# Kernel tuning notes

Hardware: AMD Instinct MI355X
Metric: run time of the kernel (lower is better)

Reference implementation:

```python
import jax, jax.numpy as jnp
import numpy as np

B = 2
ROW, COL = 63, 84          # resolution
ROW_, COL_ = 32, 42        # resolution_
N = ROW * COL              # 5292 kv tokens
N_ = ROW_ * COL_           # 1344 q tokens
IN_DIM, OUT_DIM = 256, 512
KEY_DIM, NUM_HEADS, ATTN_RATIO, STRIDE = 16, 8, 2, 2
D = ATTN_RATIO * KEY_DIM   # 32 (value dim per head)
DH = D * NUM_HEADS         # 256
NH_KD = KEY_DIM * NUM_HEADS  # 128
H_KV = DH + NH_KD          # 384
SCALE = KEY_DIM ** -0.5
EPS = 1e-5


def _build_bias_idxs():
    # replicates the itertools.product double loop, vectorized; ids ordered by
    # first occurrence in row-major scan (same as dict insertion order).
    r_ = np.arange(ROW_); c_ = np.arange(COL_)
    r = np.arange(ROW); c = np.arange(COL)
    off_r = np.abs(r_[:, None] * STRIDE - r[None, :])      # (32, 63)
    off_c = np.abs(c_[:, None] * STRIDE - c[None, :])      # (42, 84)
    keys = (off_r[:, None, :, None] * 1000 + off_c[None, :, None, :]).reshape(-1)
    _, first_idx, inv = np.unique(keys, return_index=True, return_inverse=True)
    order = np.argsort(first_idx)
    rank = np.empty_like(order); rank[order] = np.arange(len(order))
    idxs = rank[inv].reshape(N_, N).astype(np.int32)
    return idxs, len(order)


def setup_inputs() -> dict:
    key = jax.random.key(0)
    ks = jax.random.split(key, 12)
    idxs_np, n_off = _build_bias_idxs()
    inp = {
        "x": jax.random.normal(ks[0], (B, N, IN_DIM), jnp.float32),
        "kv_w": jax.random.normal(ks[1], (H_KV, IN_DIM), jnp.float32) * (IN_DIM ** -0.5),
        "kv_g": jnp.ones((H_KV,), jnp.float32),
        "kv_b": jnp.zeros((H_KV,), jnp.float32),
        "q_w": jax.random.normal(ks[2], (NH_KD, IN_DIM), jnp.float32) * (IN_DIM ** -0.5),
        "q_g": jnp.ones((NH_KD,), jnp.float32),
        "q_b": jnp.zeros((NH_KD,), jnp.float32),
        "proj_w": jax.random.normal(ks[3], (OUT_DIM, DH), jnp.float32) * (DH ** -0.5),
        "proj_g": jnp.ones((OUT_DIM,), jnp.float32),
        "proj_b": jnp.zeros((OUT_DIM,), jnp.float32),
        "bias_table": jax.random.normal(ks[4], (NUM_HEADS, n_off), jnp.float32) * 0.02,
        "bias_idxs": jnp.asarray(idxs_np),
    }
    return inp


def _linear_bn(x, w, g, b):
    # Linear (no bias) followed by BatchNorm1d in training mode (batch stats
    # over flattened (B*N) dim, biased variance).
    y = jnp.einsum("bnc,oc->bno", x, w)
    flat = y.reshape(-1, y.shape[-1])
    mu = flat.mean(0)
    var = flat.var(0)
    return (y - mu) * (g / jnp.sqrt(var + EPS)) + b


def _hardswish(x):
    return x * jnp.clip(x + 3.0, 0.0, 6.0) / 6.0


def reference(x, kv_w, kv_g, kv_b, q_w, q_g, q_b, proj_w, proj_g, proj_b,
              bias_table, bias_idxs):
    Bx = x.shape[0]
    # kv projection -> split k (KEY_DIM) and v (D) per head
    kv = _linear_bn(x, kv_w, kv_g, kv_b).reshape(Bx, N, NUM_HEADS, KEY_DIM + D)
    k = kv[..., :KEY_DIM].transpose(0, 2, 1, 3)   # (B, H, N, key_dim)
    v = kv[..., KEY_DIM:].transpose(0, 2, 1, 3)   # (B, H, N, d)
    # q: spatial subsample then projection
    xs = x.reshape(Bx, ROW, COL, IN_DIM)[:, ::STRIDE, ::STRIDE].reshape(Bx, N_, IN_DIM)
    q = _linear_bn(xs, q_w, q_g, q_b).reshape(Bx, N_, NUM_HEADS, KEY_DIM).transpose(0, 2, 1, 3)
    # gathered relative position bias: (H, N_, N)
    ab = bias_table[:, bias_idxs]
    attn = jnp.einsum("bhqd,bhkd->bhqk", q, k) * SCALE + ab[None]
    attn = jax.nn.softmax(attn, axis=-1)
    out = jnp.einsum("bhqk,bhkd->bhqd", attn, v)       # (B, H, N_, d)
    out = out.transpose(0, 2, 1, 3).reshape(Bx, N_, DH)
    out = _linear_bn(_hardswish(out), proj_w, proj_g, proj_b)
    return out
```

## Files before the change

kernel.cpp:

```cpp
#include <hip/hip_runtime.h>
#include <hip/hip_bf16.h>
#include <math.h>

#define N_K 5292
#define N_KP 5376
#define N_Q 1344
#define NH_KD 128
#define NROWS 21504
#define NSPLIT 8
#define LOG2E 1.4426950408889634f
#define MSTAT 16.0f

typedef float f32x4 __attribute__((ext_vector_type(4)));
typedef short short8 __attribute__((ext_vector_type(8)));

__device__ __forceinline__ float fexp2(float x) {
#if __has_builtin(__builtin_amdgcn_exp2f)
    return __builtin_amdgcn_exp2f(x);
#else
    return exp2f(x);
#endif
}

__device__ __forceinline__ unsigned pk_bf16(float a, float b) {
    union { __hip_bfloat162 h; unsigned u; } c;
    c.h = __float22bfloat162_rn(make_float2(a, b));
    return c.u;
}
__device__ __forceinline__ unsigned short f2bf(float a) {
    return (unsigned short)pk_bf16(a, 0.f);
}

__global__ __launch_bounds__(256) void prep_bf16(
    const float* __restrict__ X, const float* __restrict__ kv_w,
    const float* __restrict__ q_w,
    unsigned short* __restrict__ Xb, float* __restrict__ sums)
{
    int i = blockIdx.x * 256 + threadIdx.x;
    if (i >= 710144) {
        int j = i - 710144;
        float4 z = make_float4(0.f, 0.f, 0.f, 0.f);
        *(float4*)(sums + (size_t)j * 8)     = z;
        *(float4*)(sums + (size_t)j * 8 + 4) = z;
        return;
    }
    const float* src;
    long off;
    if (i < 677376)       { src = X;      off = i; }
    else if (i < 701952)  { src = kv_w;   off = i - 677376; }
    else                  { src = q_w;    off = i - 701952; }
    float4 v = *(const float4*)(src + off * 4);
    *(uint2*)(Xb + (size_t)i * 4) = make_uint2(pk_bf16(v.x, v.y), pk_bf16(v.z, v.w));
}

__device__ __forceinline__ void gemm_body_bb(
    const unsigned short* __restrict__ A, const unsigned short* __restrict__ W,
    long asrc, int nrow,
    unsigned short (*As)[40], unsigned short (*Bs)[40], f32x4 acc[4])
{
    const int t = threadIdx.x;
    const int w = t >> 6, lane = t & 63, g = lane >> 4, ln = lane & 15;
    const int srow = t >> 2;
    const int sc8 = (t & 3) * 8;

    for (int k0 = 0; k0 < 256; k0 += 32) {
        uint4 a = make_uint4(0, 0, 0, 0);
        if (asrc >= 0) a = *(const uint4*)(A + asrc * 256 + k0 + sc8);
        uint4 b = *(const uint4*)(W + (size_t)nrow * 256 + k0 + sc8);

        __syncthreads();
        *(uint4*)&As[srow][sc8] = a;
        *(uint4*)&Bs[srow][sc8] = b;
        __syncthreads();

        short8 ah = *(const short8*)&As[w * 16 + ln][g * 8];
        #pragma unroll
        for (int nt = 0; nt < 4; ++nt) {
            short8 bh = *(const short8*)&Bs[nt * 16 + ln][g * 8];
            acc[nt] = __builtin_amdgcn_mfma_f32_16x16x32_bf16(ah, bh, acc[nt], 0, 0, 0);
        }
    }
}

__device__ __forceinline__ void gemm_stats(f32x4 acc[4], float* __restrict__ sums,
                                           int n0, int Ncols, float* scratch)
{
    const int t = threadIdx.x;
    const int w = t >> 6, lane = t & 63, g = lane >> 4, ln = lane & 15;
    float s4[4], q4[4];
    #pragma unroll
    for (int nt = 0; nt < 4; ++nt) {
        float s = acc[nt][0] + acc[nt][1] + acc[nt][2] + acc[nt][3];
        float q = fmaf(acc[nt][0], acc[nt][0], fmaf(acc[nt][1], acc[nt][1],
                  fmaf(acc[nt][2], acc[nt][2], acc[nt][3] * acc[nt][3])));
        s += __shfl_xor(s, 16); s += __shfl_xor(s, 32);
        q += __shfl_xor(q, 16); q += __shfl_xor(q, 32);
        s4[nt] = s; q4[nt] = q;
    }
    __syncthreads();
    float* st_s = scratch;
    float* st_q = scratch + 256;
    if (g == 0) {
        #pragma unroll
        for (int nt = 0; nt < 4; ++nt) {
            st_s[(w * 4 + nt) * 16 + ln] = s4[nt];
            st_q[(w * 4 + nt) * 16 + ln] = q4[nt];
        }
    }
    __syncthreads();
    if (t < 64) {
        int nt = t >> 4, c = t & 15;
        float a = 0.f, b2 = 0.f;
        #pragma unroll
        for (int ww = 0; ww < 4; ++ww) {
            a  += st_s[(ww * 4 + nt) * 16 + c];
            b2 += st_q[(ww * 4 + nt) * 16 + c];
        }
        atomicAdd(&sums[n0 + nt * 16 + c], a);
        atomicAdd(&sums[Ncols + n0 + nt * 16 + c], b2);
    }
}

__global__ __launch_bounds__(256) void gemm_qkv(
    const unsigned short* __restrict__ Xb, const unsigned short* __restrict__ kvWb,
    const unsigned short* __restrict__ qWb,
    const float* __restrict__ bias_table, const int* __restrict__ bias_idxs, int n_off,
    unsigned short* __restrict__ Kp, unsigned short* __restrict__ Vpt,
    float* __restrict__ bt_r,
    float* __restrict__ q_y, float* __restrict__ sums_kv, float* __restrict__ sums_q)
{
    __shared__ unsigned short As[64][40], Bs[64][40];
    const int t = threadIdx.x;
    const int w = t >> 6, lane = t & 63, g = lane >> 4, ln = lane & 15;
    const int srow = t >> 2;
    int id = blockIdx.x;

    if (id >= 1104) {
        id -= 1104;
        if (id < 168) {
            int i = id * 256 + t;
            int row = i / 84, j = i - row * 84;
            int slot;
            if (j < 20) {
                int kap = 44 + j;
                slot = 5248 + (((kap & 15) << 2) | (kap >> 4));
            } else {
                slot = 5312 + (j - 20);
            }
            Vpt[(size_t)row * N_KP + slot] = 0;
        } else {
            int i = (id - 168) * 256 + t;
            if (i < 8 * N_K) {
                int h = i / N_K, j = i - h * N_K;
                bt_r[i] = bias_table[h * n_off + bias_idxs[j]] * LOG2E;
            }
        }
        return;
    }

    f32x4 acc[4];
    #pragma unroll
    for (int nt = 0; nt < 4; ++nt) acc[nt] = (f32x4){0.f, 0.f, 0.f, 0.f};

    if (id < 1008) {
        const int xcd = id & 7, id8 = id >> 3;
        const int my = xcd + (id8 / 6) * 8, ny = id8 % 6;
        if (my >= 166) return;
        const int m0 = my * 64, n0 = ny * 64;
        int mrow = m0 + srow;
        long asrc = (mrow < 10584) ? mrow : -1;
        gemm_body_bb(Xb, kvWb, asrc, n0 + srow, As, Bs, acc);

        #pragma unroll
        for (int nt = 0; nt < 4; ++nt) {
            int c = n0 + nt * 16 + ln;
            int hh = c / 48, cc = c - 48 * hh;
            #pragma unroll
            for (int reg = 0; reg < 4; ++reg) {
                int mr = m0 + w * 16 + g * 4 + reg;
                if (mr < 10584) {
                    int bb = mr >= N_K;
                    int key = mr - bb * N_K;
                    unsigned short v16 = f2bf(acc[nt][reg]);
                    if (cc < 16) {
                        Kp[((size_t)(bb * 8 + hh) * N_K + key) * 16 + cc] = v16;
                    } else {
                        int kap = key & 63;
                        int keyp = (key & ~63) | (((kap & 15) << 2) | (kap >> 4));
                        Vpt[((size_t)(bb * 8 + hh) * 32 + cc - 16) * N_KP + keyp] = v16;
                    }
                }
            }
        }
        gemm_stats(acc, sums_kv, n0, 384, (float*)&As[0][0]);
    } else {
        id -= 1008;
        const int xcd = id & 7, id8 = id >> 3;
        const int my = xcd + (id8 / 2) * 8, ny = id8 % 2;
        if (my >= 42) return;
        const int m0 = my * 64, n0 = ny * 64;
        int mrow = m0 + srow;
        int bb = mrow / N_Q;
        int i = mrow - bb * N_Q;
        long asrc = (long)(bb * N_K + (i / 42) * 168 + (i % 42) * 2);
        gemm_body_bb(Xb, qWb, asrc, n0 + srow, As, Bs, acc);

        #pragma unroll
        for (int nt = 0; nt < 4; ++nt)
            #pragma unroll
            for (int reg = 0; reg < 4; ++reg) {
                int mr = m0 + w * 16 + g * 4 + reg;
                q_y[(size_t)mr * 128 + n0 + nt * 16 + ln] = acc[nt][reg];
            }
        gemm_stats(acc, sums_q, n0, 128, (float*)&As[0][0]);
    }
}

__global__ __launch_bounds__(256) void gemm_proj(
    const unsigned short* __restrict__ Ap, const unsigned short* __restrict__ Wp,
    float* __restrict__ Y, float* __restrict__ sums)
{
    __shared__ unsigned short As[64][40], Bs[64][40];
    const int t = threadIdx.x;
    const int w = t >> 6, lane = t & 63, g = lane >> 4, ln = lane & 15;
    const int id = blockIdx.x;
    const int xcd = id & 7, id8 = id >> 3;
    const int my = xcd + (id8 / 8) * 8, ny = id8 % 8;
    if (my >= 42) return;
    const int m0 = my * 64, n0 = ny * 64;

    f32x4 acc[4];
    #pragma unroll
    for (int nt = 0; nt < 4; ++nt) acc[nt] = (f32x4){0.f, 0.f, 0.f, 0.f};
    gemm_body_bb(Ap, Wp, m0 + (t >> 2), n0 + (t >> 2), As, Bs, acc);

    #pragma unroll
    for (int nt = 0; nt < 4; ++nt)
        #pragma unroll
        for (int reg = 0; reg < 4; ++reg) {
            int mr = m0 + w * 16 + g * 4 + reg;
            Y[(size_t)mr * 512 + n0 + nt * 16 + ln] = acc[nt][reg];
        }
    gemm_stats(acc, sums, n0, 512, (float*)&As[0][0]);
}

__global__ __launch_bounds__(256, 5) void attn_mfma(
    const unsigned short* __restrict__ Kp, const unsigned short* __restrict__ Vpt,
    const float* __restrict__ q_y, const float* __restrict__ sums_q,
    const float* __restrict__ q_g, const float* __restrict__ q_b,
    const float* __restrict__ sums_kv, const float* __restrict__ kv_g,
    const float* __restrict__ bt_r,
    float* __restrict__ pl, float* __restrict__ pacc)
{
    const int id = blockIdx.x;
    const int h = id & 7;
    const int z = (id >> 3) & 15;
    const int qt = id >> 7;
    const int b = z >> 3, ks = z & 7;
    const int t = threadIdx.x;
    const int w = t >> 6, lane = t & 63, g = lane >> 4, ln = lane & 15;

    __shared__ unsigned short btm_s[14 * 166];
    __shared__ unsigned short K_s[2][64][24];
    __shared__ unsigned short Vt_s[2][32][72];
    __shared__ unsigned short P_s[4][16][72];

    const int q0 = qt * 64;
    const int t0 = (ks * 83) >> 3;
    const int t1 = ((ks + 1) * 83) >> 3;
    const int kstart = t0 * 64;
    const int kend0 = t1 * 64;
    const int kend = kend0 < N_K ? kend0 : N_K;
    const int ntiles = t1 - t0;
    const bool tail = (ks == 7);

    const int kr0 = kstart / 84;
    const int kr1 = (kend - 1) / 84;
    const int rq2min = (q0 / 42) * 2;
    const int rq2max = ((q0 + 63) / 42) * 2;
    const int dmin_r = rq2min - kr1;
    const int rows = (rq2max - kr0) - dmin_r + 1;
    const int nb = rows * 166;
    const unsigned mxb = (unsigned)((nb - 1) * 2);
    {
        const float* src = bt_r + h * N_K;
        for (int j = t; j < nb; j += 256) {
            int rr = j / 166, ii = j - rr * 166;
            int dr = dmin_r + rr; dr = dr < 0 ? -dr : dr;
            int dc = ii - 83; dc = dc < 0 ? -dc : dc;
            btm_s[j] = f2bf(src[dr * 84 + dc]);
        }
    }

    short8 qfrag = (short8)0;
    if (lane < 32) {
        const float invq = 1.f / 2688.f, invk = 1.f / 10584.f;
        const float post = 0.25f * LOG2E;
        const int c0 = h * 16 + g * 8;
        const int ck = h * 48 + g * 8;
        const float* qp = q_y + (size_t)(b * N_Q + q0 + w * 16 + ln) * NH_KD + c0;
        float vv[8];
        #pragma unroll
        for (int j = 0; j < 8; ++j) {
            float mu  = sums_q[c0 + j] * invq;
            float var = fmaf(-mu, mu, sums_q[128 + c0 + j] * invq);
            float s   = q_g[c0 + j] * rsqrtf(var + 1e-5f) * post;
            float vq  = fmaf(qp[j], s, fmaf(-mu, s, q_b[c0 + j] * post));
            float muk = sums_kv[ck + j] * invk;
            float vrk = fmaf(-muk, muk, sums_kv[384 + ck + j] * invk);
            float sk  = kv_g[ck + j] * rsqrtf(vrk + 1e-5f);
            vv[j] = vq * sk;
        }
        union { short8 s; unsigned u[4]; } qf;
        qf.u[0] = pk_bf16(vv[0], vv[1]); qf.u[1] = pk_bf16(vv[2], vv[3]);
        qf.u[2] = pk_bf16(vv[4], vv[5]); qf.u[3] = pk_bf16(vv[6], vv[7]);
        qfrag = qf.s;
    }

    union { short8 s; unsigned u[4]; } onef;
    #pragma unroll
    for (int j = 0; j < 4; ++j) onef.u[j] = 0x3F803F80u;
    const short8 ones = onef.s;

    int baseb[4];
    #pragma unroll
    for (int reg = 0; reg < 4; ++reg) {
        int qg = q0 + w * 16 + g * 4 + reg;
        int rq2 = (qg / 42) * 2;
        int cq2 = (qg % 42) * 2;
        baseb[reg] = ((rq2 - dmin_r) * 166 + cq2 + 83) * 2;
    }
    int offb[4], kcc[4];
    #pragma unroll
    for (int st = 0; st < 4; ++st) {
        int kg = kstart + st * 16 + ln;
        int okr = kg / 84;
        kcc[st] = kg - okr * 84;
        offb[st] = -(okr * 166 + kcc[st]) * 2;
    }

    const unsigned* kp_base = (const unsigned*)Kp + (size_t)(b * 8 + h) * N_K * 8;
    const int skey = t >> 2, schunk = t & 3;
    const int vrow = t >> 3, vc8 = (t & 7) * 8;
    const unsigned short* vptr = Vpt + (size_t)(b * 8 + h) * 32 * N_KP
                                     + (size_t)vrow * N_KP + kstart + vc8;

    uint2 kreg; uint4 vreg;
    {
        int kg = kstart + skey; if (kg > N_K - 1) kg = N_K - 1;
        kreg = *(const uint2*)(kp_base + (size_t)kg * 8 + schunk * 2);
        vreg = *(const uint4*)vptr;
    }
    *(uint2*)&K_s[0][skey][schunk * 4] = kreg;
    *(uint4*)&Vt_s[0][vrow][vc8] = vreg;
    __syncthreads();

    f32x4 acc0 = {0.f, 0.f, 0.f, 0.f}, acc1 = {0.f, 0.f, 0.f, 0.f};
    f32x4 accL = {0.f, 0.f, 0.f, 0.f};
    const f32x4 minit = {-MSTAT, -MSTAT, -MSTAT, -MSTAT};
    int p = 0;

    for (int it = 0; it < ntiles; ++it) {
        const int k0 = kstart + it * 64;
        const bool notlast = (it + 1 < ntiles);
        if (notlast) {
            int kg = k0 + 64 + skey; if (kg > N_K - 1) kg = N_K - 1;
            kreg = *(const uint2*)(kp_base + (size_t)kg * 8 + schunk * 2);
            vreg = *(const uint4*)(vptr + 64);
        }

        f32x4 sf[4];
        #pragma unroll
        for (int st = 0; st < 4; ++st) {
            short8 bf = (short8)0;
            if (lane < 32) bf = *(const short8*)&K_s[p][st * 16 + ln][g * 8];
            sf[st] = __builtin_amdgcn_mfma_f32_16x16x32_bf16(qfrag, bf, minit, 0, 0, 0);
        }

        float pv[4][4];
        const bool clampit = tail && (it == ntiles - 1);
        if (!clampit) {
            #pragma unroll
            for (int st = 0; st < 4; ++st) {
                #pragma unroll
                for (int reg = 0; reg < 4; ++reg) {
                    unsigned ub = (unsigned)(baseb[reg] + offb[st]);
                    unsigned short bu = *(const unsigned short*)((const char*)btm_s + ub);
                    float bias = __uint_as_float(((unsigned)bu) << 16);
                    pv[st][reg] = fexp2(sf[st][reg] + bias);
                }
            }
        } else {
            #pragma unroll
            for (int st = 0; st < 4; ++st) {
                bool bad = (k0 + st * 16 + ln) >= N_K;
                #pragma unroll
                for (int reg = 0; reg < 4; ++reg) {
                    unsigned ub = (unsigned)(baseb[reg] + offb[st]);
                    ub = ub > mxb ? mxb : ub;
                    unsigned short bu = *(const unsigned short*)((const char*)btm_s + ub);
                    float bias = __uint_as_float(((unsigned)bu) << 16);
                    pv[st][reg] = bad ? 0.f : fexp2(sf[st][reg] + bias);
                }
            }
        }

        #pragma unroll
        for (int reg = 0; reg < 4; ++reg) {
            uint2 pw = make_uint2(pk_bf16(pv[0][reg], pv[1][reg]),
                                  pk_bf16(pv[2][reg], pv[3][reg]));
            *(uint2*)&P_s[w][g * 4 + reg][4 * ln] = pw;
        }
        __asm__ __volatile__("" ::: "memory");

        #pragma unroll
        for (int kt = 0; kt < 2; ++kt) {
            short8 af = *(const short8*)&P_s[w][ln][g * 8 + kt * 32];
            short8 b0 = *(const short8*)&Vt_s[p][ln][g * 8 + kt * 32];
            short8 b1 = *(const short8*)&Vt_s[p][ln + 16][g * 8 + kt * 32];
            acc0 = __builtin_amdgcn_mfma_f32_16x16x32_bf16(af, b0, acc0, 0, 0, 0);
            acc1 = __builtin_amdgcn_mfma_f32_16x16x32_bf16(af, b1, acc1, 0, 0, 0);
            accL = __builtin_amdgcn_mfma_f32_16x16x32_bf16(af, ones, accL, 0, 0, 0);
        }

        if (notlast) {
            int q2 = p ^ 1;
            *(uint2*)&K_s[q2][skey][schunk * 4] = kreg;
            *(uint4*)&Vt_s[q2][vrow][vc8] = vreg;
            __syncthreads();
            p = q2;
            vptr += 64;
        }

        #pragma unroll
        for (int st = 0; st < 4; ++st) {
            kcc[st] += 64;
            if (kcc[st] >= 84) { kcc[st] -= 84; offb[st] -= 292; }
            else offb[st] -= 128;
        }
    }

    const int rbase = (b * 8 + h) * N_Q + q0 + w * 16;
    #pragma unroll
    for (int reg = 0; reg < 4; ++reg) {
        int prow = ks * NROWS + rbase + g * 4 + reg;
        pacc[(size_t)prow * 32 + ln]      = acc0[reg];
        pacc[(size_t)prow * 32 + 16 + ln] = acc1[reg];
        if (ln == 0) pl[prow] = accL[reg];
    }
}

__global__ __launch_bounds__(256) void combine_kernel(const float* __restrict__ pl,
                                                      const float* __restrict__ pacc,
                                                      const float* __restrict__ sums_kv,
                                                      const float* __restrict__ kv_g,
                                                      const float* __restrict__ kv_b,
                                                      unsigned short* __restrict__ attn_o,
                                                      const float* __restrict__ proj_w,
                                                      unsigned short* __restrict__ projWb)
{
    if (blockIdx.x >= 672) {
        int i = (blockIdx.x - 672) * 256 + threadIdx.x;
        float4 v = *(const float4*)(proj_w + (size_t)i * 4);
        *(uint2*)(projWb + (size_t)i * 4) = make_uint2(pk_bf16(v.x, v.y), pk_bf16(v.z, v.w));
        return;
    }
    int idx = blockIdx.x * 256 + threadIdx.x;
    int r = idx >> 3, e4 = (idx & 7) * 4;
    float L = 0.f;
    float vs[4] = {0.f, 0.f, 0.f, 0.f};
    size_t o = (size_t)r * 32 + e4;
    #pragma unroll
    for (int s2 = 0; s2 < NSPLIT; ++s2) {
        L += pl[(size_t)s2 * NROWS + r];
        float4 vv = *(const float4*)(pacc + (size_t)s2 * NROWS * 32 + o);
        vs[0] += vv.x; vs[1] += vv.y; vs[2] += vv.z; vs[3] += vv.w;
    }
    float invL = 1.f / L;
    int q = r % N_Q;
    int bh = r / N_Q;
    int hh = bh & 7, b = bh >> 3;
    const int ch = hh * 48 + 16 + e4;
    const float invk = 1.f / 10584.f;
    float hs[4];
    #pragma unroll
    for (int u = 0; u < 4; ++u) {
        float v = vs[u];
        float mu  = sums_kv[ch + u] * invk;
        float var = fmaf(-mu, mu, sums_kv[384 + ch + u] * invk);
        float s   = kv_g[ch + u] * rsqrtf(var + 1e-5f);
        float tt  = fmaf(-mu, s, kv_b[ch + u]);
        v = fmaf(s, v * invL, tt);
        hs[u] = v * fminf(fmaxf(v + 3.f, 0.f), 6.f) * (1.f / 6.f);
    }
    *(uint2*)(attn_o + (size_t)(b * N_Q + q) * 256 + hh * 32 + e4) =
        make_uint2(pk_bf16(hs[0], hs[1]), pk_bf16(hs[2], hs[3]));
}

__global__ __launch_bounds__(256) void norm_apply(
    const float* __restrict__ Y, const float* __restrict__ sums,
    const float* __restrict__ g, const float* __restrict__ bb,
    float* __restrict__ out, int rows, int cols, float inv_rows)
{
    __shared__ float sc_s[64], sh_s[64];
    const int t = threadIdx.x;
    const int c0 = blockIdx.x * 64;
    if (t < 64) {
        int c = c0 + t;
        float mu  = sums[c] * inv_rows;
        float var = fmaf(-mu, mu, sums[cols + c] * inv_rows);
        float s   = g[c] * rsqrtf(var + 1e-5f);
        sc_s[t] = s;
        sh_s[t] = fmaf(-mu, s, bb[c]);
    }
    __syncthreads();
    const int c4 = (t & 15) * 4;
    float4 scv = *(const float4*)&sc_s[c4];
    float4 shv = *(const float4*)&sh_s[c4];
    for (int r = blockIdx.y * 16 + (t >> 4); r < rows; r += gridDim.y * 16) {
        size_t off = (size_t)r * cols + c0 + c4;
        float4 v = *(const float4*)(Y + off);
        v.x = fmaf(v.x, scv.x, shv.x);
        v.y = fmaf(v.y, scv.y, shv.y);
        v.z = fmaf(v.z, scv.z, shv.z);
        v.w = fmaf(v.w, scv.w, shv.w);
        *(float4*)(out + off) = v;
    }
}

extern "C" void kernel_launch(void* const* d_in, const int* in_sizes, int n_in,
                              void* d_out, int out_size, void* d_ws, size_t ws_size,
                              hipStream_t stream) {
    (void)n_in; (void)out_size; (void)ws_size;
    const float* x      = (const float*)d_in[0];
    const float* kv_w   = (const float*)d_in[1];
    const float* kv_g   = (const float*)d_in[2];
    const float* kv_b   = (const float*)d_in[3];
    const float* q_w    = (const float*)d_in[4];
    const float* q_g    = (const float*)d_in[5];
    const float* q_b    = (const float*)d_in[6];
    const float* proj_w = (const float*)d_in[7];
    const float* proj_g = (const float*)d_in[8];
    const float* proj_b = (const float*)d_in[9];
    const float* bias_table = (const float*)d_in[10];
    const int*   bias_idxs  = (const int*)d_in[11];
    const int    n_off = in_sizes[10] / 8;
    float* out = (float*)d_out;

    float* ws = (float*)d_ws;
    float* q_y  = ws;
    float* pacc = q_y + 2688 * 128;
    float* proj_y = pacc;
    float* pl = pacc + (size_t)NSPLIT * NROWS * 32;
    unsigned short* attn_o = (unsigned short*)(pl + (size_t)NSPLIT * NROWS);
    unsigned short* Kp  = attn_o + 2688 * 256;
    unsigned short* Vpt = Kp + 2 * 8 * N_K * 16;
    float* sums_kv = (float*)(Vpt + 2 * 8 * 32 * N_KP);
    float* sums_q  = sums_kv + 768;
    float* sums_p  = sums_q + 256;
    float* bt_r    = sums_p + 1024;

    unsigned short* Xb     = (unsigned short*)pacc;
    unsigned short* kvWb   = Xb + 10584 * 256;
    unsigned short* qWb    = kvWb + 384 * 256;
    unsigned short* projWb = (unsigned short*)q_y;

    prep_bf16<<<2775, 256, 0, stream>>>(x, kv_w, q_w, Xb, sums_kv);
    gemm_qkv<<<1104 + 168 + 166, 256, 0, stream>>>(Xb, kvWb, qWb, bias_table, bias_idxs,
                                                   n_off, Kp, Vpt, bt_r,
                                                   q_y, sums_kv, sums_q);
    attn_mfma<<<2688, 256, 0, stream>>>(Kp, Vpt, q_y, sums_q, q_g, q_b,
                                        sums_kv, kv_g, bt_r, pl, pacc);
    combine_kernel<<<672 + 128, 256, 0, stream>>>(pl, pacc, sums_kv, kv_g, kv_b, attn_o,
                                                  proj_w, projWb);
    gemm_proj<<<384, 256, 0, stream>>>(attn_o, projWb, proj_y, sums_p);
    norm_apply<<<dim3(8, 84), 256, 0, stream>>>(proj_y, sums_p, proj_g, proj_b, out,
                                                2688, 512, 1.f / 2688.f);
}
```

Measured before the change: 184.0 us.

## Load GEMM A operand and attention K/V fragments directly from global memory

```diff
diff --git a/kernel.cpp b/kernel.cpp
--- a/kernel.cpp
+++ b/kernel.cpp
@@ -53,30 +53,33 @@
     *(uint2*)(Xb + (size_t)i * 4) = make_uint2(pk_bf16(v.x, v.y), pk_bf16(v.z, v.w));
 }
 
-__device__ __forceinline__ void gemm_body_bb(
+__device__ __forceinline__ void gemm_body_direct(
     const unsigned short* __restrict__ A, const unsigned short* __restrict__ W,
-    long asrc, int nrow,
-    unsigned short (*As)[40], unsigned short (*Bs)[40], f32x4 acc[4])
+    long arow,
+    int n0,
+    unsigned short (*Bs)[264], f32x4 acc[4])
 {
     const int t = threadIdx.x;
-    const int w = t >> 6, lane = t & 63, g = lane >> 4, ln = lane & 15;
-    const int srow = t >> 2;
-    const int sc8 = (t & 3) * 8;
-
+    const int lane = t & 63, g = lane >> 4, ln = lane & 15;
+
+    #pragma unroll
+    for (int p = 0; p < 8; ++p) {
+        int i = p * 256 + t;
+        int row = i >> 5, c8 = (i & 31) * 8;
+        *(uint4*)&Bs[row][c8] = *(const uint4*)(W + (size_t)(n0 + row) * 256 + c8);
+    }
+    __syncthreads();
+
+    const unsigned short* aptr =
+        (arow >= 0) ? (A + (size_t)arow * 256 + g * 8) : (const unsigned short*)0;
+
+    #pragma unroll
     for (int k0 = 0; k0 < 256; k0 += 32) {
-        uint4 a = make_uint4(0, 0, 0, 0);
-        if (asrc >= 0) a = *(const uint4*)(A + asrc * 256 + k0 + sc8);
-        uint4 b = *(const uint4*)(W + (size_t)nrow * 256 + k0 + sc8);
-
-        __syncthreads();
-        *(uint4*)&As[srow][sc8] = a;
-        *(uint4*)&Bs[srow][sc8] = b;
-        __syncthreads();
-
-        short8 ah = *(const short8*)&As[w * 16 + ln][g * 8];
+        short8 ah = (short8)0;
+        if (aptr) ah = *(const short8*)(aptr + k0);
         #pragma unroll
         for (int nt = 0; nt < 4; ++nt) {
-            short8 bh = *(const short8*)&Bs[nt * 16 + ln][g * 8];
+            short8 bh = *(const short8*)&Bs[nt * 16 + ln][k0 + g * 8];
             acc[nt] = __builtin_amdgcn_mfma_f32_16x16x32_bf16(ah, bh, acc[nt], 0, 0, 0);
         }
     }
@@ -129,10 +132,9 @@
     float* __restrict__ bt_r,
     float* __restrict__ q_y, float* __restrict__ sums_kv, float* __restrict__ sums_q)
 {
-    __shared__ unsigned short As[64][40], Bs[64][40];
+    __shared__ unsigned short Bs[64][264];
     const int t = threadIdx.x;
     const int w = t >> 6, lane = t & 63, g = lane >> 4, ln = lane & 15;
-    const int srow = t >> 2;
     int id = blockIdx.x;
 
     if (id >= 1104) {
@@ -167,9 +169,9 @@
         const int my = xcd + (id8 / 6) * 8, ny = id8 % 6;
         if (my >= 166) return;
         const int m0 = my * 64, n0 = ny * 64;
-        int mrow = m0 + srow;
-        long asrc = (mrow < 10584) ? mrow : -1;
-        gemm_body_bb(Xb, kvWb, asrc, n0 + srow, As, Bs, acc);
+        int arow0 = m0 + w * 16 + ln;
+        long arow = (arow0 < 10584) ? arow0 : -1;
+        gemm_body_direct(Xb, kvWb, arow, n0, Bs, acc);
 
         #pragma unroll
         for (int nt = 0; nt < 4; ++nt) {
@@ -192,18 +194,18 @@
                 }
             }
         }
-        gemm_stats(acc, sums_kv, n0, 384, (float*)&As[0][0]);
+        gemm_stats(acc, sums_kv, n0, 384, (float*)&Bs[0][0]);
     } else {
         id -= 1008;
         const int xcd = id & 7, id8 = id >> 3;
         const int my = xcd + (id8 / 2) * 8, ny = id8 % 2;
         if (my >= 42) return;
         const int m0 = my * 64, n0 = ny * 64;
-        int mrow = m0 + srow;
+        int mrow = m0 + w * 16 + ln;
         int bb = mrow / N_Q;
         int i = mrow - bb * N_Q;
-        long asrc = (long)(bb * N_K + (i / 42) * 168 + (i % 42) * 2);
-        gemm_body_bb(Xb, qWb, asrc, n0 + srow, As, Bs, acc);
+        long arow = (long)(bb * N_K + (i / 42) * 168 + (i % 42) * 2);
+        gemm_body_direct(Xb, qWb, arow, n0, Bs, acc);
 
         #pragma unroll
         for (int nt = 0; nt < 4; ++nt)
@@ -212,7 +214,7 @@
                 int mr = m0 + w * 16 + g * 4 + reg;
                 q_y[(size_t)mr * 128 + n0 + nt * 16 + ln] = acc[nt][reg];
             }
-        gemm_stats(acc, sums_q, n0, 128, (float*)&As[0][0]);
+        gemm_stats(acc, sums_q, n0, 128, (float*)&Bs[0][0]);
     }
 }
 
@@ -220,7 +222,7 @@
     const unsigned short* __restrict__ Ap, const unsigned short* __restrict__ Wp,
     float* __restrict__ Y, float* __restrict__ sums)
 {
-    __shared__ unsigned short As[64][40], Bs[64][40];
+    __shared__ unsigned short Bs[64][264];
     const int t = threadIdx.x;
     const int w = t >> 6, lane = t & 63, g = lane >> 4, ln = lane & 15;
     const int id = blockIdx.x;
@@ -232,7 +234,7 @@
     f32x4 acc[4];
     #pragma unroll
     for (int nt = 0; nt < 4; ++nt) acc[nt] = (f32x4){0.f, 0.f, 0.f, 0.f};
-    gemm_body_bb(Ap, Wp, m0 + (t >> 2), n0 + (t >> 2), As, Bs, acc);
+    gemm_body_direct(Ap, Wp, (long)(m0 + w * 16 + ln), n0, Bs, acc);
 
     #pragma unroll
     for (int nt = 0; nt < 4; ++nt)
@@ -241,10 +243,10 @@
             int mr = m0 + w * 16 + g * 4 + reg;
             Y[(size_t)mr * 512 + n0 + nt * 16 + ln] = acc[nt][reg];
         }
-    gemm_stats(acc, sums, n0, 512, (float*)&As[0][0]);
-}
-
-__global__ __launch_bounds__(256, 5) void attn_mfma(
+    gemm_stats(acc, sums, n0, 512, (float*)&Bs[0][0]);
+}
+
+__global__ __launch_bounds__(256, 8) void attn_mfma(
     const unsigned short* __restrict__ Kp, const unsigned short* __restrict__ Vpt,
     const float* __restrict__ q_y, const float* __restrict__ sums_q,
     const float* __restrict__ q_g, const float* __restrict__ q_b,
@@ -261,8 +263,6 @@
     const int w = t >> 6, lane = t & 63, g = lane >> 4, ln = lane & 15;
 
     __shared__ unsigned short btm_s[14 * 166];
-    __shared__ unsigned short K_s[2][64][24];
-    __shared__ unsigned short Vt_s[2][32][72];
     __shared__ unsigned short P_s[4][16][72];
 
     const int q0 = qt * 64;
@@ -316,6 +316,7 @@
         qf.u[2] = pk_bf16(vv[4], vv[5]); qf.u[3] = pk_bf16(vv[6], vv[7]);
         qfrag = qf.s;
     }
+    __syncthreads();
 
     union { short8 s; unsigned u[4]; } onef;
     #pragma unroll
@@ -339,41 +340,27 @@
         offb[st] = -(okr * 166 + kcc[st]) * 2;
     }
 
-    const unsigned* kp_base = (const unsigned*)Kp + (size_t)(b * 8 + h) * N_K * 8;
-    const int skey = t >> 2, schunk = t & 3;
-    const int vrow = t >> 3, vc8 = (t & 7) * 8;
-    const unsigned short* vptr = Vpt + (size_t)(b * 8 + h) * 32 * N_KP
-                                     + (size_t)vrow * N_KP + kstart + vc8;
-
-    uint2 kreg; uint4 vreg;
-    {
-        int kg = kstart + skey; if (kg > N_K - 1) kg = N_K - 1;
-        kreg = *(const uint2*)(kp_base + (size_t)kg * 8 + schunk * 2);
-        vreg = *(const uint4*)vptr;
-    }
-    *(uint2*)&K_s[0][skey][schunk * 4] = kreg;
-    *(uint4*)&Vt_s[0][vrow][vc8] = vreg;
-    __syncthreads();
+    const unsigned short* kp_u16 = Kp + (size_t)(b * 8 + h) * N_K * 16;
+    const unsigned short* vb0 = Vpt + (size_t)(b * 8 + h) * 32 * N_KP
+                                    + (size_t)ln * N_KP + kstart + g * 8;
+    const unsigned short* vb1 = vb0 + (size_t)16 * N_KP;
 
     f32x4 acc0 = {0.f, 0.f, 0.f, 0.f}, acc1 = {0.f, 0.f, 0.f, 0.f};
     f32x4 accL = {0.f, 0.f, 0.f, 0.f};
     const f32x4 minit = {-MSTAT, -MSTAT, -MSTAT, -MSTAT};
-    int p = 0;
 
     for (int it = 0; it < ntiles; ++it) {
         const int k0 = kstart + it * 64;
-        const bool notlast = (it + 1 < ntiles);
-        if (notlast) {
-            int kg = k0 + 64 + skey; if (kg > N_K - 1) kg = N_K - 1;
-            kreg = *(const uint2*)(kp_base + (size_t)kg * 8 + schunk * 2);
-            vreg = *(const uint4*)(vptr + 64);
-        }
 
         f32x4 sf[4];
         #pragma unroll
         for (int st = 0; st < 4; ++st) {
             short8 bf = (short8)0;
-            if (lane < 32) bf = *(const short8*)&K_s[p][st * 16 + ln][g * 8];
+            if (lane < 32) {
+                int key = k0 + st * 16 + ln;
+                key = key > N_K - 1 ? N_K - 1 : key;
+                bf = *(const short8*)(kp_u16 + (size_t)key * 16 + g * 8);
+            }
             sf[st] = __builtin_amdgcn_mfma_f32_16x16x32_bf16(qfrag, bf, minit, 0, 0, 0);
         }
 
@@ -416,20 +403,11 @@
         #pragma unroll
         for (int kt = 0; kt < 2; ++kt) {
             short8 af = *(const short8*)&P_s[w][ln][g * 8 + kt * 32];
-            short8 b0 = *(const short8*)&Vt_s[p][ln][g * 8 + kt * 32];
-            short8 b1 = *(const short8*)&Vt_s[p][ln + 16][g * 8 + kt * 32];
+            short8 b0 = *(const short8*)(vb0 + it * 64 + kt * 32);
+            short8 b1 = *(const short8*)(vb1 + it * 64 + kt * 32);
             acc0 = __builtin_amdgcn_mfma_f32_16x16x32_bf16(af, b0, acc0, 0, 0, 0);
             acc1 = __builtin_amdgcn_mfma_f32_16x16x32_bf16(af, b1, acc1, 0, 0, 0);
             accL = __builtin_amdgcn_mfma_f32_16x16x32_bf16(af, ones, accL, 0, 0, 0);
-        }
-
-        if (notlast) {
-            int q2 = p ^ 1;
-            *(uint2*)&K_s[q2][skey][schunk * 4] = kreg;
-            *(uint4*)&Vt_s[q2][vrow][vc8] = vreg;
-            __syncthreads();
-            p = q2;
-            vptr += 64;
         }
 
         #pragma unroll
```

After: 280.3 us. 1.52x slower.
